# Kernel tuning notes

Hardware: AMD Instinct MI355X
Metric: run time of the kernel (lower is better)

The kernel has to match this reference:

```python
import jax, jax.numpy as jnp
import numpy as np

NUM_TOKENS = 128
STRING_SIZE = 512
HIDDEN_SIZE = 2048
L_IN = 256
L_OUT = 256
MAX_PROGRAM_LENGTH = 10


def _lstm_scan(xs, h, c, Wih, Whh, b):
    """Run a PyTorch-convention LSTM (gate order i,f,g,o) over xs [L, D]."""
    def step(carry, x):
        h, c = carry
        g = x @ Wih.T + h @ Whh.T + b          # [4H]
        i, f, gg, o = jnp.split(g, 4)
        c2 = jax.nn.sigmoid(f) * c + jax.nn.sigmoid(i) * jnp.tanh(gg)
        h2 = jax.nn.sigmoid(o) * jnp.tanh(c2)
        return (h2, c2), None
    (h, c), _ = jax.lax.scan(step, (h, c), xs)
    return h, c


def setup_inputs() -> dict:
    key = jax.random.key(0)
    ks = jax.random.split(key, 13)
    H, S = HIDDEN_SIZE, STRING_SIZE
    def p(k, shape, scale=0.02):
        return scale * jax.random.normal(k, shape, dtype=jnp.float32)
    return {
        "input_sequence": jax.random.randint(ks[0], (L_IN,), 0, NUM_TOKENS),
        "output_sequence": jax.random.randint(ks[1], (L_OUT,), 0, NUM_TOKENS),
        "embed": p(ks[2], (NUM_TOKENS, S), 1.0),
        "eos": p(ks[3], (S,), 1.0),
        "in_Wih": p(ks[4], (4 * H, S)), "in_Whh": p(ks[5], (4 * H, H)), "in_b": p(ks[6], (4 * H,)),
        "out_Wih": p(ks[7], (4 * H, S)), "out_Whh": p(ks[8], (4 * H, H)), "out_b": p(ks[9], (4 * H,)),
        "prog_Wih": p(ks[10], (4 * H, H)), "prog_Whh": p(ks[11], (4 * H, H)), "prog_b": p(ks[12], (4 * H,)),
    }


def reference(input_sequence, output_sequence, embed, eos,
              in_Wih, in_Whh, in_b, out_Wih, out_Whh, out_b,
              prog_Wih, prog_Whh, prog_b):
    H = in_Whh.shape[1]
    h = jnp.zeros((H,), embed.dtype)
    c = jnp.zeros((H,), embed.dtype)
    # encode input string (+ end-of-sequence token) with input_lstm
    xs_in = jnp.concatenate([embed[input_sequence], eos[None]], axis=0)   # [L_in+1, S]
    h, c = _lstm_scan(xs_in, h, c, in_Wih, in_Whh, in_b)
    # encode output string (+ eos) with output_lstm, state carried over
    xs_out = jnp.concatenate([embed[output_sequence], eos[None]], axis=0)  # [L_out+1, S]
    h, c = _lstm_scan(xs_out, h, c, out_Wih, out_Whh, out_b)
    def prog_step(carry, _):
        h, c = carry
        g = h @ prog_Wih.T + h @ prog_Whh.T + prog_b
        i, f, gg, o = jnp.split(g, 4)
        c2 = jax.nn.sigmoid(f) * c + jax.nn.sigmoid(i) * jnp.tanh(gg)
        h2 = jax.nn.sigmoid(o) * jnp.tanh(c2)
        return (h2, c2), h2
    _, prog = jax.lax.scan(prog_step, (h, c), None, length=MAX_PROGRAM_LENGTH)
    return prog  # [MAX_PROGRAM_LENGTH, H] (stack of program hidden states)
```

## Files before the change

### kernel.cpp

```cpp
#include <hip/hip_runtime.h>

typedef unsigned short u16;
typedef unsigned int u32;
typedef unsigned long long u64;

#define NBLK 256
#define XR 544

__device__ __forceinline__ float b2f(u16 u) {
    u32 i = ((u32)u) << 16;
    return __builtin_bit_cast(float, i);
}
__device__ __forceinline__ u16 f2b(float f) {
    u32 b = __builtin_bit_cast(u32, f);
    b += 0x7FFFu + ((b >> 16) & 1u);
    return (u16)(b >> 16);
}
__device__ __forceinline__ float sigm(float x) {
    return 1.f / (1.f + __expf(-x));
}
__device__ __forceinline__ float tanh_fast(float x) {
    float a = fabsf(x);
    float e = __expf(-2.f * a);
    float r = (1.f - e) / (1.f + e);
    return copysignf(r, x);
}

__global__ void __launch_bounds__(256)
xproj_kernel(const float* __restrict__ embed, const float* __restrict__ eos,
             const int* __restrict__ seqA, const int* __restrict__ seqB,
             const float* __restrict__ WA, const float* __restrict__ WB,
             const float* __restrict__ bA, const float* __restrict__ bB,
             float* __restrict__ XpA, float* __restrict__ XpB)
{
    __shared__ __align__(16) float xs[8 * XR];
    const int which = blockIdx.x >> 8;
    const int bx = blockIdx.x & 255;
    const int* __restrict__ seq  = which ? seqB : seqA;
    const float* __restrict__ W  = which ? WB : WA;
    const float* __restrict__ bias = which ? bB : bA;
    float* __restrict__ Xp = which ? XpB : XpA;

    const int tid = threadIdx.x;
    const int lane = tid & 63;
    const int wv = tid >> 6;
    const int row = lane & 7;
    const int seg = lane >> 3;

    const int r = bx * 32 + wv * 8 + row;
    float4 w4[16];
    {
        const float* wp = &W[(size_t)r * 512 + seg * 64];
#pragma unroll
        for (int c = 0; c < 16; ++c) w4[c] = *(const float4*)&wp[c * 4];
    }
    const float brow = bias[r];
    const int g = r >> 11, rem = r & 2047;
    const int slot = ((rem >> 3) << 5) + (g << 3) + (rem & 7);

    for (int grp = 0; grp < 33; ++grp) {
        const int t0 = grp * 8;
        const int nt = min(8, 257 - t0);
        __syncthreads();
        for (int idx = tid; idx < nt * 512; idx += 256) {
            int tt = idx >> 9, col = idx & 511;
            int tk = t0 + tt;
            float v = (tk < 256) ? embed[(size_t)seq[tk] * 512 + col] : eos[col];
            xs[tt * XR + col + ((col >> 6) << 2)] = v;
        }
        __syncthreads();

#pragma unroll 1
        for (int tt = 0; tt < 8; ++tt) {
            const float* xrow = &xs[tt * XR + seg * 68];
            float a = 0.f;
#pragma unroll
            for (int c = 0; c < 16; ++c) {
                float4 xv = *(const float4*)&xrow[c * 4];
                a = fmaf(w4[c].x, xv.x, a);
                a = fmaf(w4[c].y, xv.y, a);
                a = fmaf(w4[c].z, xv.z, a);
                a = fmaf(w4[c].w, xv.w, a);
            }
            a += __shfl_xor(a, 8, 64);
            a += __shfl_xor(a, 16, 64);
            a += __shfl_xor(a, 32, 64);
            if (lane < 8 && tt < nt)
                Xp[(size_t)(t0 + tt) * 8192 + slot] = a + brow;
        }
    }
}

__global__ void __launch_bounds__(512, 1)
rnn_coop(const float* __restrict__ WhhA, const float* __restrict__ WhhB,
         const float* __restrict__ pWih, const float* __restrict__ pWhh,
         const float* __restrict__ pB,
         const float* __restrict__ Xp0, const float* __restrict__ Xp1,
         u32* __restrict__ hseqB, float* __restrict__ out)
{
    __shared__ __align__(16) float hs[2048];
    __shared__ float gsum[32];

    const int wg = blockIdx.x;
    const int tid = threadIdx.x;
    const int lane = tid & 63;
    const int wv = tid >> 6;

    float w[4][32];
    float c_reg = 0.f;

    if (tid < 32) gsum[tid] = 0.f;

    float xp_cur = 0.f, xp_nxt = 0.f;
    if (wv == 0 && lane < 32)
        xp_cur = Xp0[(size_t)0 * 8192 + (wg << 5) + lane];

    for (int t = 0; t < 524; ++t) {
        const int phase = (t < 257) ? 0 : (t < 514) ? 1 : 2;

        if (t == 0 || t == 257 || t == 514) {
            if (phase < 2) {
                const float* Ws = phase ? WhhB : WhhA;
#pragma unroll
                for (int rr = 0; rr < 4; ++rr) {
                    int rl = (wv << 2) + rr;
                    const float* Wr = Ws + (size_t)(((rl >> 3) << 11) + (wg << 3) + (rl & 7)) * 2048;
#pragma unroll
                    for (int q = 0; q < 8; ++q)
                        *(float4*)&w[rr][q * 4] = *(const float4*)&Wr[(q << 8) + (lane << 2)];
                }
            } else {
#pragma unroll
                for (int rr = 0; rr < 4; ++rr) {
                    int rl = (wv << 2) + rr;
                    size_t off = (size_t)(((rl >> 3) << 11) + (wg << 3) + (rl & 7)) * 2048;
#pragma unroll
                    for (int q = 0; q < 8; ++q) {
                        float4 a = *(const float4*)&pWih[off + (q << 8) + (lane << 2)];
                        float4 b = *(const float4*)&pWhh[off + (q << 8) + (lane << 2)];
                        float4 s;
                        s.x = a.x + b.x; s.y = a.y + b.y;
                        s.z = a.z + b.z; s.w = a.w + b.w;
                        *(float4*)&w[rr][q * 4] = s;
                    }
                }
            }
        }

        if (t > 0) {
            const u64* src = (const u64*)hseqB + (size_t)(t - 1) * 512 + tid;
            u64 a = __hip_atomic_load(src, __ATOMIC_RELAXED, __HIP_MEMORY_SCOPE_AGENT);
            while ((u16)a == 0xFFFFu || (u16)(a >> 16) == 0xFFFFu ||
                   (u16)(a >> 32) == 0xFFFFu || (u16)(a >> 48) == 0xFFFFu)
                a = __hip_atomic_load(src, __ATOMIC_RELAXED, __HIP_MEMORY_SCOPE_AGENT);
            float4 hv;
            hv.x = b2f((u16)a);         hv.y = b2f((u16)(a >> 16));
            hv.z = b2f((u16)(a >> 32)); hv.w = b2f((u16)(a >> 48));
            *(float4*)&hs[tid << 2] = hv;
        }
        __syncthreads();

        if (wv == 0 && lane < 32 && t < 523) {
            const int tn = t + 1;
            if (tn < 257)       xp_nxt = Xp0[(size_t)tn * 8192 + (wg << 5) + lane];
            else if (tn < 514)  xp_nxt = Xp1[(size_t)(tn - 257) * 8192 + (wg << 5) + lane];
            else                xp_nxt = pB[((lane >> 3) << 11) + (wg << 3) + (lane & 7)];
        }

        if (t > 0) {
            float a0 = 0.f, a1 = 0.f, a2 = 0.f, a3 = 0.f;
#pragma unroll
            for (int q = 0; q < 8; ++q) {
                float4 hv = *(const float4*)&hs[(q << 8) + (lane << 2)];
#pragma unroll
                for (int j = 0; j < 4; ++j) {
                    float h = ((const float*)&hv)[j];
                    a0 = fmaf(w[0][q * 4 + j], h, a0);
                    a1 = fmaf(w[1][q * 4 + j], h, a1);
                    a2 = fmaf(w[2][q * 4 + j], h, a2);
                    a3 = fmaf(w[3][q * 4 + j], h, a3);
                }
            }
#pragma unroll
            for (int off = 32; off > 0; off >>= 1) {
                a0 += __shfl_xor(a0, off, 64);
                a1 += __shfl_xor(a1, off, 64);
                a2 += __shfl_xor(a2, off, 64);
                a3 += __shfl_xor(a3, off, 64);
            }
            if (lane == 0) {
                const int rl = wv << 2;
                gsum[rl]     = a0;
                gsum[rl + 1] = a1;
                gsum[rl + 2] = a2;
                gsum[rl + 3] = a3;
            }
        }
        __syncthreads();

        if (wv == 0) {
            float tot = xp_cur + gsum[lane & 31];
            float act = ((lane >> 3) == 2) ? tanh_fast(tot) : sigm(tot);
            const int j = lane & 7;
            float fi = __shfl(act, j, 64);
            float ff = __shfl(act, 8 + j, 64);
            float fg = __shfl(act, 16 + j, 64);
            float fo = __shfl(act, 24 + j, 64);
            c_reg = ff * c_reg + fi * fg;
            float h2 = fo * tanh_fast(c_reg);
            u32 hb = (u32)f2b(h2);
            u32 lo = (u32)__shfl((int)hb, (lane & 3) * 2, 64);
            u32 hi = (u32)__shfl((int)hb, (lane & 3) * 2 + 1, 64);
            if (lane < 4)
                __hip_atomic_store(&hseqB[(size_t)t * 1024 + (wg << 2) + lane],
                                   (hi << 16) | lo,
                                   __ATOMIC_RELAXED, __HIP_MEMORY_SCOPE_AGENT);
            if (phase == 2 && lane < 8)
                out[(size_t)(t - 514) * 2048 + (wg << 3) + lane] = h2;
        }
        xp_cur = xp_nxt;
    }
}

extern "C" void kernel_launch(void* const* d_in, const int* in_sizes, int n_in,
                              void* d_out, int out_size, void* d_ws, size_t ws_size,
                              hipStream_t stream) {
    const int*   in_seq   = (const int*)d_in[0];
    const int*   out_seq  = (const int*)d_in[1];
    const float* embed    = (const float*)d_in[2];
    const float* eos      = (const float*)d_in[3];
    const float* in_Wih   = (const float*)d_in[4];
    const float* in_Whh   = (const float*)d_in[5];
    const float* in_b     = (const float*)d_in[6];
    const float* out_Wih  = (const float*)d_in[7];
    const float* out_Whh  = (const float*)d_in[8];
    const float* out_b    = (const float*)d_in[9];
    const float* pg_Wih   = (const float*)d_in[10];
    const float* pg_Whh   = (const float*)d_in[11];
    const float* pg_b     = (const float*)d_in[12];

    float* Xp0   = (float*)d_ws;
    float* Xp1   = Xp0 + (size_t)257 * 8192;
    u32*   hseqB = (u32*)(Xp1 + (size_t)257 * 8192);

    hipMemsetAsync(hseqB, 0xFF, (size_t)524 * 1024 * sizeof(u32), stream);

    hipLaunchKernelGGL(xproj_kernel, dim3(512), dim3(256), 0, stream,
                       embed, eos, in_seq, out_seq,
                       in_Wih, out_Wih, in_b, out_b, Xp0, Xp1);

    float* out = (float*)d_out;
    void* args[] = { (void*)&in_Whh, (void*)&out_Whh, (void*)&pg_Wih, (void*)&pg_Whh,
                     (void*)&pg_b, (void*)&Xp0, (void*)&Xp1, (void*)&hseqB, (void*)&out };
    hipLaunchCooperativeKernel((const void*)rnn_coop, dim3(NBLK), dim3(512),
                               args, 0, stream);
}
```

Baseline: 1.908 ms.

## Fuse input projection into cooperative RNN kernel prologue

Removes the separate xproj kernel launch. Each cooperative workgroup now computes the input-projection slots it later consumes itself, in a prologue before the recurrent loop. This removes a kernel launch and the boundary between the two kernels. In exchange, the persistent kernel uses an extra shared-memory buffer and a different thread mapping for the projection (two timestep halves per workgroup).

```diff
diff --git a/kernel.cpp b/kernel.cpp
--- a/kernel.cpp
+++ b/kernel.cpp
@@ -26,78 +26,18 @@
     return copysignf(r, x);
 }
 
-__global__ void __launch_bounds__(256)
-xproj_kernel(const float* __restrict__ embed, const float* __restrict__ eos,
-             const int* __restrict__ seqA, const int* __restrict__ seqB,
-             const float* __restrict__ WA, const float* __restrict__ WB,
-             const float* __restrict__ bA, const float* __restrict__ bB,
-             float* __restrict__ XpA, float* __restrict__ XpB)
-{
-    __shared__ __align__(16) float xs[8 * XR];
-    const int which = blockIdx.x >> 8;
-    const int bx = blockIdx.x & 255;
-    const int* __restrict__ seq  = which ? seqB : seqA;
-    const float* __restrict__ W  = which ? WB : WA;
-    const float* __restrict__ bias = which ? bB : bA;
-    float* __restrict__ Xp = which ? XpB : XpA;
-
-    const int tid = threadIdx.x;
-    const int lane = tid & 63;
-    const int wv = tid >> 6;
-    const int row = lane & 7;
-    const int seg = lane >> 3;
-
-    const int r = bx * 32 + wv * 8 + row;
-    float4 w4[16];
-    {
-        const float* wp = &W[(size_t)r * 512 + seg * 64];
-#pragma unroll
-        for (int c = 0; c < 16; ++c) w4[c] = *(const float4*)&wp[c * 4];
-    }
-    const float brow = bias[r];
-    const int g = r >> 11, rem = r & 2047;
-    const int slot = ((rem >> 3) << 5) + (g << 3) + (rem & 7);
-
-    for (int grp = 0; grp < 33; ++grp) {
-        const int t0 = grp * 8;
-        const int nt = min(8, 257 - t0);
-        __syncthreads();
-        for (int idx = tid; idx < nt * 512; idx += 256) {
-            int tt = idx >> 9, col = idx & 511;
-            int tk = t0 + tt;
-            float v = (tk < 256) ? embed[(size_t)seq[tk] * 512 + col] : eos[col];
-            xs[tt * XR + col + ((col >> 6) << 2)] = v;
-        }
-        __syncthreads();
-
-#pragma unroll 1
-        for (int tt = 0; tt < 8; ++tt) {
-            const float* xrow = &xs[tt * XR + seg * 68];
-            float a = 0.f;
-#pragma unroll
-            for (int c = 0; c < 16; ++c) {
-                float4 xv = *(const float4*)&xrow[c * 4];
-                a = fmaf(w4[c].x, xv.x, a);
-                a = fmaf(w4[c].y, xv.y, a);
-                a = fmaf(w4[c].z, xv.z, a);
-                a = fmaf(w4[c].w, xv.w, a);
-            }
-            a += __shfl_xor(a, 8, 64);
-            a += __shfl_xor(a, 16, 64);
-            a += __shfl_xor(a, 32, 64);
-            if (lane < 8 && tt < nt)
-                Xp[(size_t)(t0 + tt) * 8192 + slot] = a + brow;
-        }
-    }
-}
-
 __global__ void __launch_bounds__(512, 1)
 rnn_coop(const float* __restrict__ WhhA, const float* __restrict__ WhhB,
          const float* __restrict__ pWih, const float* __restrict__ pWhh,
          const float* __restrict__ pB,
-         const float* __restrict__ Xp0, const float* __restrict__ Xp1,
+         const float* __restrict__ inWih, const float* __restrict__ outWih,
+         const float* __restrict__ in_b, const float* __restrict__ out_b,
+         const float* __restrict__ embed, const float* __restrict__ eos,
+         const int* __restrict__ in_seq, const int* __restrict__ out_seq,
+         float* __restrict__ Xp0, float* __restrict__ Xp1,
          u32* __restrict__ hseqB, float* __restrict__ out)
 {
+    __shared__ __align__(16) float xs[8 * XR];
     __shared__ __align__(16) float hs[2048];
     __shared__ float gsum[32];
 
@@ -106,6 +46,67 @@
     const int lane = tid & 63;
     const int wv = tid >> 6;
 
+    {
+        const int g = wv & 3;
+        const int th = wv >> 2;
+        const int j = lane & 7;
+        const int seg = lane >> 3;
+        const int r = (g << 11) + (wg << 3) + j;
+        const int slot = (wg << 5) + (g << 3) + j;
+
+        for (int p = 0; p < 2; ++p) {
+            const float* __restrict__ Wih = p ? outWih : inWih;
+            const float* __restrict__ bia = p ? out_b : in_b;
+            const int*   __restrict__ sq  = p ? out_seq : in_seq;
+            float* __restrict__ Xp = p ? Xp1 : Xp0;
+
+            float4 w4[16];
+            {
+                const float* wp = &Wih[(size_t)r * 512 + seg * 64];
+#pragma unroll
+                for (int c = 0; c < 16; ++c) w4[c] = *(const float4*)&wp[c * 4];
+            }
+            const float brow = bia[r];
+
+            for (int grp = 0; grp < 33; ++grp) {
+                const int t0 = grp * 8;
+                const int nt = min(8, 257 - t0);
+                __syncthreads();
+                for (int idx = tid; idx < nt * 512; idx += 512) {
+                    int tt = idx >> 9, col = idx & 511;
+                    int tk = t0 + tt;
+                    float v = (tk < 256) ? embed[(size_t)sq[tk] * 512 + col]
+                                         : eos[col];
+                    xs[tt * XR + col + ((col >> 6) << 2)] = v;
+                }
+                __syncthreads();
+
+#pragma unroll
+                for (int q4 = 0; q4 < 4; ++q4) {
+                    const int tt = th * 4 + q4;
+                    if (tt < nt) {
+                        const float* xrow = &xs[tt * XR + seg * 68];
+                        float a = 0.f;
+#pragma unroll
+                        for (int c = 0; c < 16; ++c) {
+                            float4 xv = *(const float4*)&xrow[c * 4];
+                            a = fmaf(w4[c].x, xv.x, a);
+                            a = fmaf(w4[c].y, xv.y, a);
+                            a = fmaf(w4[c].z, xv.z, a);
+                            a = fmaf(w4[c].w, xv.w, a);
+                        }
+                        a += __shfl_xor(a, 8, 64);
+                        a += __shfl_xor(a, 16, 64);
+                        a += __shfl_xor(a, 32, 64);
+                        if (lane < 8)
+                            Xp[(size_t)(t0 + tt) * 8192 + slot] = a + brow;
+                    }
+                }
+            }
+        }
+        __syncthreads();
+    }
+
     float w[4][32];
     float c_reg = 0.f;
 
@@ -113,7 +114,7 @@
 
     float xp_cur = 0.f, xp_nxt = 0.f;
     if (wv == 0 && lane < 32)
-        xp_cur = Xp0[(size_t)0 * 8192 + (wg << 5) + lane];
+        xp_cur = Xp0[(wg << 5) + lane];
 
     for (int t = 0; t < 524; ++t) {
         const int phase = (t < 257) ? 0 : (t < 514) ? 1 : 2;
@@ -245,13 +246,12 @@
 
     hipMemsetAsync(hseqB, 0xFF, (size_t)524 * 1024 * sizeof(u32), stream);
 
-    hipLaunchKernelGGL(xproj_kernel, dim3(512), dim3(256), 0, stream,
-                       embed, eos, in_seq, out_seq,
-                       in_Wih, out_Wih, in_b, out_b, Xp0, Xp1);
-
     float* out = (float*)d_out;
     void* args[] = { (void*)&in_Whh, (void*)&out_Whh, (void*)&pg_Wih, (void*)&pg_Whh,
-                     (void*)&pg_b, (void*)&Xp0, (void*)&Xp1, (void*)&hseqB, (void*)&out };
+                     (void*)&pg_b,
+                     (void*)&in_Wih, (void*)&out_Wih, (void*)&in_b, (void*)&out_b,
+                     (void*)&embed, (void*)&eos, (void*)&in_seq, (void*)&out_seq,
+                     (void*)&Xp0, (void*)&Xp1, (void*)&hseqB, (void*)&out };
     hipLaunchCooperativeKernel((const void*)rnn_coop, dim3(NBLK), dim3(512),
                                args, 0, stream);
 }
```

Measured after the change: 1.811 ms. 5.1% less time.
